# Kernel tuning notes

Measured on AMD Instinct MI355X. Metric: run time of the kernel, lower is better.

Reference implementation:

```python
import jax, jax.numpy as jnp
import numpy as np

N_NODES = 100000
N_EDGES = 1600000
IN_FEAT = 64
HIDDEN = 64
OUT_FEAT = 64
FCHIDDEN = 32
EMB_DIM = 20
FINAL_DIM = 2


def gcn_conv(x, W, b, src, dst, num_nodes):
    """PyG-style GCNConv: add self-loops, symmetric norm, linear, scatter-add."""
    loop = jnp.arange(num_nodes)
    s = jnp.concatenate([src, loop])  # message sources (x_j)
    d = jnp.concatenate([dst, loop])  # aggregation targets
    ones = jnp.ones(s.shape[0], dtype=x.dtype)
    deg = jax.ops.segment_sum(ones, d, num_segments=num_nodes)
    dinv = jnp.where(deg > 0, jax.lax.rsqrt(jnp.maximum(deg, 1.0)), 0.0)
    norm = dinv[s] * dinv[d]                      # [E+N]
    h = x @ W                                     # [N, out]
    msg = h[s] * norm[:, None]                    # gather + scale
    return jax.ops.segment_sum(msg, d, num_segments=num_nodes) + b


def setup_inputs() -> dict:
    key = jax.random.key(0)
    ks = jax.random.split(key, 12)
    x = jax.random.normal(ks[0], (N_NODES, IN_FEAT), dtype=jnp.float32)
    edge_index = jax.random.randint(ks[1], (2, N_EDGES), 0, N_NODES, dtype=jnp.int64)
    edge_attr = jax.random.randint(ks[2], (4, N_EDGES), 0, EMB_DIM, dtype=jnp.int64)
    def lin(k, fan_in, fan_out):
        bound = 1.0 / np.sqrt(fan_in)
        kw, kb = jax.random.split(k)
        W = jax.random.uniform(kw, (fan_in, fan_out), jnp.float32, -bound, bound)
        b = jax.random.uniform(kb, (fan_out,), jnp.float32, -bound, bound)
        return W, b
    W1, b1 = lin(ks[3], IN_FEAT, HIDDEN)
    W2, b2 = lin(ks[4], HIDDEN, OUT_FEAT)
    emb0 = jax.random.normal(ks[5], (EMB_DIM, FCHIDDEN), dtype=jnp.float32)
    emb1 = jax.random.normal(ks[6], (EMB_DIM, FCHIDDEN), dtype=jnp.float32)
    fc_in = OUT_FEAT + 2 * FCHIDDEN + 2
    fcW1, fcb1 = lin(ks[7], fc_in, FINAL_DIM)
    fcW2, fcb2 = lin(ks[8], FINAL_DIM, 2)
    return dict(x=x, edge_index=edge_index, edge_attr=edge_attr,
                W1=W1, b1=b1, W2=W2, b2=b2, emb0=emb0, emb1=emb1,
                fcW1=fcW1, fcb1=fcb1, fcW2=fcW2, fcb2=fcb2)


def reference(x, edge_index, edge_attr, W1, b1, W2, b2, emb0, emb1,
              fcW1, fcb1, fcW2, fcb2):
    num_nodes = x.shape[0]
    src, dst = edge_index[0], edge_index[1]
    h = jax.nn.relu(gcn_conv(x, W1, b1, src, dst, num_nodes))
    h = gcn_conv(h, W2, b2, src, dst, num_nodes)
    node2edge = h[src] - h[dst]                     # [E, outFeat]
    ea = edge_attr.T                                # [E, 4]
    vl = ea[:, :2].astype(jnp.float32)              # [E, 2]
    e0 = emb0[ea[:, 2]]                             # [E, fchidden]
    e1 = emb1[ea[:, 3]]                             # [E, fchidden]
    total = jnp.concatenate([node2edge, vl, e0, e1], axis=1)
    out = jax.nn.relu(total @ fcW1 + fcb1)          # dropout = identity (eval)
    out = out @ fcW2 + fcb2                         # [E, 2]
    return jax.nn.log_softmax(out, axis=1)
```

## Files before the change

kernel.cpp:

```cpp
#include <hip/hip_runtime.h>
#include <hip/hip_bf16.h>
#include <math.h>


typedef __hip_bfloat16 bf16;
#define NBLK 256

__global__ __launch_bounds__(256) void kA(const int* __restrict__ dst,
                                          int* __restrict__ cntm,
                                          int E, int chunk, int NB) {
    __shared__ int h[512];
    int blk = blockIdx.x;
    for (int i = threadIdx.x; i < NB; i += 256) h[i] = 0;
    __syncthreads();
    int lo = blk * chunk, hi = min(E, lo + chunk);
    for (int e = lo + threadIdx.x; e < hi; e += 256)
        atomicAdd(&h[dst[e] >> 8], 1);
    __syncthreads();
    for (int i = threadIdx.x; i < NB; i += 256)
        cntm[(size_t)i * NBLK + blk] = h[i];
}

__global__ void k_mscan1(int* __restrict__ a, int* __restrict__ part, int M) {
    __shared__ int s[256];
    int i = blockIdx.x * 256 + threadIdx.x;
    int v = (i < M) ? a[i] : 0;
    s[threadIdx.x] = v;
    int x = v;
    for (int off = 1; off < 256; off <<= 1) {
        __syncthreads();
        int add = (threadIdx.x >= off) ? s[threadIdx.x - off] : 0;
        __syncthreads();
        x += add;
        s[threadIdx.x] = x;
    }
    if (i < M) a[i] = x - v;
    __syncthreads();
    if (threadIdx.x == 255) part[blockIdx.x] = s[255];
}

__global__ __launch_bounds__(512) void k_scan2small(
        int* __restrict__ part, int B,
        const float* __restrict__ W2,
        const float* __restrict__ emb0, const float* __restrict__ emb1,
        const float* __restrict__ fcW1, const float* __restrict__ fcb1,
        const float* __restrict__ fcW2, const float* __restrict__ fcb2,
        float* __restrict__ U, float* __restrict__ E0t,
        float* __restrict__ E1t, float* __restrict__ C) {
    __shared__ int s[512];
    int t = threadIdx.x;
    int v = (t < B) ? part[t] : 0;
    s[t] = v;
    int x = v;
    for (int off = 1; off < 512; off <<= 1) {
        __syncthreads();
        int add = (t >= off) ? s[t - off] : 0;
        __syncthreads();
        x += add;
        s[t] = x;
    }
    if (t < B) part[t] = x - v;
    if (t < 128) {
        int i = t >> 1, c = t & 1;
        float sum = 0.f;
        for (int j = 0; j < 64; ++j) sum += W2[i * 64 + j] * fcW1[j * 2 + c];
        U[i * 2 + c] = sum;
    } else if (t < 168) {
        int i = (t - 128) >> 1, c = t & 1;
        float s0 = 0.f, s1 = 0.f;
        for (int k = 0; k < 32; ++k) {
            s0 += emb0[i * 32 + k] * fcW1[(66 + k) * 2 + c];
            s1 += emb1[i * 32 + k] * fcW1[(98 + k) * 2 + c];
        }
        E0t[i * 2 + c] = s0;
        E1t[i * 2 + c] = s1;
    } else if (t == 168) {
        C[0] = fcb1[0];  C[1] = fcb1[1];
        C[2] = fcW1[128]; C[3] = fcW1[129];
        C[4] = fcW1[130]; C[5] = fcW1[131];
        C[6] = fcW2[0];  C[7] = fcW2[1];
        C[8] = fcW2[2];  C[9] = fcW2[3];
        C[10] = fcb2[0]; C[11] = fcb2[1];
    }
}

__global__ __launch_bounds__(256) void kB(const int* __restrict__ src,
                                          const int* __restrict__ dst,
                                          const int* __restrict__ cntm,
                                          const int* __restrict__ part,
                                          int* __restrict__ pairs,
                                          int E, int chunk, int NB) {
    __shared__ int off[512];
    int blk = blockIdx.x;
    for (int i = threadIdx.x; i < NB; i += 256)
        off[i] = cntm[(size_t)i * NBLK + blk] + part[i];
    __syncthreads();
    int lo = blk * chunk, hi = min(E, lo + chunk);
    for (int e = lo + threadIdx.x; e < hi; e += 256) {
        int d = dst[e];
        int pos = atomicAdd(&off[d >> 8], 1);
        pairs[pos] = ((d & 255) << 17) | src[e];
    }
}

__global__ __launch_bounds__(256) void kC(const int* __restrict__ part,
                                          const int* __restrict__ pairs,
                                          int* __restrict__ col, int* __restrict__ rp,
                                          float* __restrict__ dinv,
                                          int N, int E, int NB) {
    __shared__ int cnt[256];
    __shared__ int s[256];
    int b = blockIdx.x, t = threadIdx.x;
    int n0 = b << 8;
    int nn = min(256, N - n0);
    int base = part[b];
    int end  = (b == NB - 1) ? E : part[b + 1];
    cnt[t] = 0;
    __syncthreads();
    for (int j = base + t; j < end; j += 256)
        atomicAdd(&cnt[pairs[j] >> 17], 1);
    __syncthreads();
    int v = cnt[t];
    if (t < nn) dinv[n0 + t] = rsqrtf((float)v + 1.0f);
    s[t] = v;
    int x = v;
    for (int off = 1; off < 256; off <<= 1) {
        __syncthreads();
        int add = (t >= off) ? s[t - off] : 0;
        __syncthreads();
        x += add;
        s[t] = x;
    }
    __syncthreads();
    int excl = x - v;
    if (t < nn) rp[n0 + t] = base + excl;
    cnt[t] = base + excl;
    __syncthreads();
    for (int j = base + t; j < end; j += 256) {
        int v2 = pairs[j];
        int pos = atomicAdd(&cnt[v2 >> 17], 1);
        col[pos] = v2 & 0x1FFFF;
    }
    if (b == NB - 1 && t == 0) rp[N] = E;
}

__global__ __launch_bounds__(256) void k_gemm1(const float* __restrict__ x,
                                               const float* __restrict__ W1,
                                               const float* __restrict__ dinv,
                                               bf16* __restrict__ xWs, int N) {
    __shared__ __align__(16) float xs[64][66];
    __shared__ __align__(16) float Ws[64][64];
    int tid = threadIdx.x;
    int n0 = blockIdx.x * 64;
    for (int i = tid; i < 4096; i += 256) Ws[i >> 6][i & 63] = W1[i];
    for (int i = tid; i < 4096; i += 256) {
        int node = i >> 6, k = i & 63;
        float v = (n0 + node < N) ? x[(size_t)(n0 + node) * 64 + k] : 0.f;
        xs[k][node] = v;
    }
    __syncthreads();
    int tr = tid >> 4;
    int tc = tid & 15;
    float acc[4][4] = {};
#pragma unroll 8
    for (int k = 0; k < 64; ++k) {
        float2 xa = *(const float2*)&xs[k][tr * 4];
        float2 xb = *(const float2*)&xs[k][tr * 4 + 2];
        float4 wv = *(const float4*)&Ws[k][tc * 4];
        acc[0][0] = fmaf(xa.x, wv.x, acc[0][0]);
        acc[0][1] = fmaf(xa.x, wv.y, acc[0][1]);
        acc[0][2] = fmaf(xa.x, wv.z, acc[0][2]);
        acc[0][3] = fmaf(xa.x, wv.w, acc[0][3]);
        acc[1][0] = fmaf(xa.y, wv.x, acc[1][0]);
        acc[1][1] = fmaf(xa.y, wv.y, acc[1][1]);
        acc[1][2] = fmaf(xa.y, wv.z, acc[1][2]);
        acc[1][3] = fmaf(xa.y, wv.w, acc[1][3]);
        acc[2][0] = fmaf(xb.x, wv.x, acc[2][0]);
        acc[2][1] = fmaf(xb.x, wv.y, acc[2][1]);
        acc[2][2] = fmaf(xb.x, wv.z, acc[2][2]);
        acc[2][3] = fmaf(xb.x, wv.w, acc[2][3]);
        acc[3][0] = fmaf(xb.y, wv.x, acc[3][0]);
        acc[3][1] = fmaf(xb.y, wv.y, acc[3][1]);
        acc[3][2] = fmaf(xb.y, wv.z, acc[3][2]);
        acc[3][3] = fmaf(xb.y, wv.w, acc[3][3]);
    }
#pragma unroll
    for (int i = 0; i < 4; ++i) {
        int node = n0 + tr * 4 + i;
        if (node < N) {
            float di = dinv[node];
            __hip_bfloat162 p0, p1;
            p0.x = __float2bfloat16(di * acc[i][0]);
            p0.y = __float2bfloat16(di * acc[i][1]);
            p1.x = __float2bfloat16(di * acc[i][2]);
            p1.y = __float2bfloat16(di * acc[i][3]);
            __hip_bfloat162* dst2 = (__hip_bfloat162*)&xWs[(size_t)node * 64 + tc * 4];
            dst2[0] = p0;
            dst2[1] = p1;
        }
    }
}

__global__ __launch_bounds__(256) void k_gather1(
        const bf16* __restrict__ xWs, const float* __restrict__ dinv,
        const int* __restrict__ rp, const int* __restrict__ col,
        const float* __restrict__ b1, const float* __restrict__ U,
        float* __restrict__ Qs, int N, int E) {
    int wid = blockIdx.x * 8 + (threadIdx.x >> 5);
    int c = threadIdx.x & 31;
    if (wid >= N) return;
    const __hip_bfloat162* xW2 = (const __hip_bfloat162*)xWs;
    __hip_bfloat162 sv = xW2[(size_t)wid * 32 + c];
    float ax = __bfloat162float(sv.x);
    float ay = __bfloat162float(sv.y);
    int beg = rp[wid], end = rp[wid + 1];
    for (int base = beg; base < end; base += 32) {
        int nn = min(32, end - base);
        int colv = col[min(base + c, E - 1)];
        int jj = 0;
        for (; jj + 8 <= nn; jj += 8) {
            int m0 = __shfl(colv, jj + 0, 32);
            int m1 = __shfl(colv, jj + 1, 32);
            int m2 = __shfl(colv, jj + 2, 32);
            int m3 = __shfl(colv, jj + 3, 32);
            int m4 = __shfl(colv, jj + 4, 32);
            int m5 = __shfl(colv, jj + 5, 32);
            int m6 = __shfl(colv, jj + 6, 32);
            int m7 = __shfl(colv, jj + 7, 32);
            __hip_bfloat162 v0 = xW2[(size_t)m0 * 32 + c];
            __hip_bfloat162 v1 = xW2[(size_t)m1 * 32 + c];
            __hip_bfloat162 v2 = xW2[(size_t)m2 * 32 + c];
            __hip_bfloat162 v3 = xW2[(size_t)m3 * 32 + c];
            __hip_bfloat162 v4 = xW2[(size_t)m4 * 32 + c];
            __hip_bfloat162 v5 = xW2[(size_t)m5 * 32 + c];
            __hip_bfloat162 v6 = xW2[(size_t)m6 * 32 + c];
            __hip_bfloat162 v7 = xW2[(size_t)m7 * 32 + c];
            ax += __bfloat162float(v0.x); ay += __bfloat162float(v0.y);
            ax += __bfloat162float(v1.x); ay += __bfloat162float(v1.y);
            ax += __bfloat162float(v2.x); ay += __bfloat162float(v2.y);
            ax += __bfloat162float(v3.x); ay += __bfloat162float(v3.y);
            ax += __bfloat162float(v4.x); ay += __bfloat162float(v4.y);
            ax += __bfloat162float(v5.x); ay += __bfloat162float(v5.y);
            ax += __bfloat162float(v6.x); ay += __bfloat162float(v6.y);
            ax += __bfloat162float(v7.x); ay += __bfloat162float(v7.y);
        }
        for (; jj < nn; ++jj) {
            int m = __shfl(colv, jj, 32);
            __hip_bfloat162 v = xW2[(size_t)m * 32 + c];
            ax += __bfloat162float(v.x);
            ay += __bfloat162float(v.y);
        }
    }
    float di = dinv[wid];
    float2 b1v = ((const float2*)b1)[c];
    float h0 = fmaxf(fmaf(di, ax, b1v.x), 0.f);
    float h1 = fmaxf(fmaf(di, ay, b1v.y), 0.f);
    float4 Uv = ((const float4*)U)[c];
    float q0 = fmaf(h0, Uv.x, h1 * Uv.z);
    float q1 = fmaf(h0, Uv.y, h1 * Uv.w);
#pragma unroll
    for (int mm = 16; mm; mm >>= 1) {
        q0 += __shfl_xor(q0, mm);
        q1 += __shfl_xor(q1, mm);
    }
    if (c == 0) {
        Qs[2 * wid + 0] = di * q0;
        Qs[2 * wid + 1] = di * q1;
    }
}

__global__ void k_gather2(const float* __restrict__ dinv, const int* __restrict__ rp,
                          const int* __restrict__ col, const float* __restrict__ Qs,
                          float* __restrict__ P, int N) {
    int n = blockIdx.x * blockDim.x + threadIdx.x;
    if (n >= N) return;
    float2 self = ((const float2*)Qs)[n];
    float p0 = self.x, p1 = self.y;
    int beg = rp[n], end = rp[n + 1];
    int j = beg;
    for (; j + 4 <= end; j += 4) {
        int m0 = col[j + 0], m1 = col[j + 1], m2 = col[j + 2], m3 = col[j + 3];
        float2 q0 = ((const float2*)Qs)[m0];
        float2 q1 = ((const float2*)Qs)[m1];
        float2 q2 = ((const float2*)Qs)[m2];
        float2 q3 = ((const float2*)Qs)[m3];
        p0 += (q0.x + q1.x) + (q2.x + q3.x);
        p1 += (q0.y + q1.y) + (q2.y + q3.y);
    }
    for (; j < end; ++j) {
        float2 q = ((const float2*)Qs)[col[j]];
        p0 += q.x;
        p1 += q.y;
    }
    float di = dinv[n];
    P[2 * n + 0] = di * p0;
    P[2 * n + 1] = di * p1;
}

__global__ void k_edge(const int* __restrict__ src, const int* __restrict__ dst,
                       const int* __restrict__ attr, const float* __restrict__ P,
                       const float* __restrict__ E0t, const float* __restrict__ E1t,
                       const float* __restrict__ C, float* __restrict__ out, int E) {
    int e = blockIdx.x * blockDim.x + threadIdx.x;
    if (e >= E) return;
    int s = src[e], d = dst[e];
    float a0 = (float)attr[e];
    float a1 = (float)attr[E + e];
    int i2 = attr[2 * E + e], i3 = attr[3 * E + e];
    const float2* P2 = (const float2*)P;
    float2 ps = P2[s], pd = P2[d];
    float z0 = ps.x - pd.x + a0 * C[2] + a1 * C[4] + E0t[i2 * 2 + 0] + E1t[i3 * 2 + 0] + C[0];
    float z1 = ps.y - pd.y + a0 * C[3] + a1 * C[5] + E0t[i2 * 2 + 1] + E1t[i3 * 2 + 1] + C[1];
    float r0 = fmaxf(z0, 0.f), r1 = fmaxf(z1, 0.f);
    float o0 = r0 * C[6] + r1 * C[8] + C[10];
    float o1 = r0 * C[7] + r1 * C[9] + C[11];
    float m = fmaxf(o0, o1);
    float lse = m + logf(expf(o0 - m) + expf(o1 - m));
    float2 res;
    res.x = o0 - lse;
    res.y = o1 - lse;
    ((float2*)out)[e] = res;
}

extern "C" void kernel_launch(void* const* d_in, const int* in_sizes, int n_in,
                              void* d_out, int out_size, void* d_ws, size_t ws_size,
                              hipStream_t stream) {
    const float* x    = (const float*)d_in[0];
    const int*   ei   = (const int*)d_in[1];
    const int*   ea   = (const int*)d_in[2];
    const float* W1   = (const float*)d_in[3];
    const float* b1   = (const float*)d_in[4];
    const float* W2   = (const float*)d_in[5];
    const float* emb0 = (const float*)d_in[7];
    const float* emb1 = (const float*)d_in[8];
    const float* fcW1 = (const float*)d_in[9];
    const float* fcb1 = (const float*)d_in[10];
    const float* fcW2 = (const float*)d_in[11];
    const float* fcb2 = (const float*)d_in[12];

    const int N = in_sizes[0] / 64;
    const int E = in_sizes[1] / 2;
    const int* src = ei;
    const int* dst = ei + E;
    const int NB = (N + 255) >> 8;
    const int NBB = NB * NBLK;
    const int chunk = (E + NBLK - 1) / NBLK;
    const int BS = (NBB + 255) / 256;

    char* wsb = (char*)d_ws;
    float* dinv = (float*)wsb;
    int*   rp   = (int*)(wsb + (size_t)4 * 100352);
    int*   cntm = (int*)(wsb + (size_t)4 * 200704);
    int*   part = (int*)(wsb + (size_t)4 * 300800);
    float* U    = (float*)(wsb + (size_t)4 * 301312);
    float* E0t  = U + 128;
    float* E1t  = E0t + 40;
    float* C    = E1t + 40;
    float* Qs   = (float*)(wsb + (size_t)4 * 301568);
    float* P    = (float*)(wsb + (size_t)4 * 501760);
    bf16*  xWs  = (bf16*)(wsb + (size_t)4 * 702464);
    int*   col   = (int*)d_out;
    int*   pairs = (int*)d_out + E;

    kA<<<NBLK, 256, 0, stream>>>(dst, cntm, E, chunk, NB);
    k_mscan1<<<BS, 256, 0, stream>>>(cntm, part, NBB);
    k_scan2small<<<1, 512, 0, stream>>>(part, BS, W2, emb0, emb1, fcW1, fcb1,
                                        fcW2, fcb2, U, E0t, E1t, C);
    kB<<<NBLK, 256, 0, stream>>>(src, dst, cntm, part, pairs, E, chunk, NB);
    kC<<<NB, 256, 0, stream>>>(part, pairs, col, rp, dinv, N, E, NB);
    k_gemm1<<<(N + 63) / 64, 256, 0, stream>>>(x, W1, dinv, xWs, N);
    k_gather1<<<(N + 7) / 8, 256, 0, stream>>>(xWs, dinv, rp, col, b1, U, Qs, N, E);
    k_gather2<<<(N + 255) / 256, 256, 0, stream>>>(dinv, rp, col, Qs, P, N);
    k_edge<<<(E + 255) / 256, 256, 0, stream>>>(src, dst, ea, P, E0t, E1t, C,
                                                (float*)d_out, E);
}
```

Baseline: 257.1 us.

## Replace two-level bucket CSR build with global-atomic degree count and scatter

Replaces the block-histogram bucket sort (kA/kB/kC with a pairs staging buffer) with a direct CSR build: global atomic degree count, a per-node scan, a fixup kernel that also computes dinv and initialises cursors, and an atomic scatter of src into col. This removes the intermediate pairs pass and the local-sort kernel but relies on heavily contended global atomics on random destinations. Column order within a row becomes nondeterministic, and the cursor array reuses the Qs buffer before gather1 writes it.

New measurement: 404.0 us. 1.57x slower.

```diff
diff --git a/kernel.cpp b/kernel.cpp
--- a/kernel.cpp
+++ b/kernel.cpp
@@ -4,27 +4,19 @@
 
 
 typedef __hip_bfloat16 bf16;
-#define NBLK 256
-
-__global__ __launch_bounds__(256) void kA(const int* __restrict__ dst,
-                                          int* __restrict__ cntm,
-                                          int E, int chunk, int NB) {
-    __shared__ int h[512];
-    int blk = blockIdx.x;
-    for (int i = threadIdx.x; i < NB; i += 256) h[i] = 0;
-    __syncthreads();
-    int lo = blk * chunk, hi = min(E, lo + chunk);
-    for (int e = lo + threadIdx.x; e < hi; e += 256)
-        atomicAdd(&h[dst[e] >> 8], 1);
-    __syncthreads();
-    for (int i = threadIdx.x; i < NB; i += 256)
-        cntm[(size_t)i * NBLK + blk] = h[i];
-}
-
-__global__ void k_mscan1(int* __restrict__ a, int* __restrict__ part, int M) {
+
+__global__ __launch_bounds__(256) void k_deg(const int* __restrict__ dst,
+                                             int* __restrict__ deg, int E) {
+    int e = blockIdx.x * 256 + threadIdx.x;
+    if (e < E) atomicAdd(&deg[dst[e]], 1);
+}
+
+__global__ __launch_bounds__(256) void k_scan_deg(const int* __restrict__ deg,
+                                                  int* __restrict__ rp,
+                                                  int* __restrict__ part, int M) {
     __shared__ int s[256];
     int i = blockIdx.x * 256 + threadIdx.x;
-    int v = (i < M) ? a[i] : 0;
+    int v = (i < M) ? deg[i] : 0;
     s[threadIdx.x] = v;
     int x = v;
     for (int off = 1; off < 256; off <<= 1) {
@@ -34,7 +26,7 @@
         x += add;
         s[threadIdx.x] = x;
     }
-    if (i < M) a[i] = x - v;
+    if (i < M) rp[i] = x - v;
     __syncthreads();
     if (threadIdx.x == 255) part[blockIdx.x] = s[255];
 }
@@ -84,64 +76,32 @@
     }
 }
 
-__global__ __launch_bounds__(256) void kB(const int* __restrict__ src,
-                                          const int* __restrict__ dst,
-                                          const int* __restrict__ cntm,
-                                          const int* __restrict__ part,
-                                          int* __restrict__ pairs,
-                                          int E, int chunk, int NB) {
-    __shared__ int off[512];
-    int blk = blockIdx.x;
-    for (int i = threadIdx.x; i < NB; i += 256)
-        off[i] = cntm[(size_t)i * NBLK + blk] + part[i];
-    __syncthreads();
-    int lo = blk * chunk, hi = min(E, lo + chunk);
-    for (int e = lo + threadIdx.x; e < hi; e += 256) {
-        int d = dst[e];
-        int pos = atomicAdd(&off[d >> 8], 1);
-        pairs[pos] = ((d & 255) << 17) | src[e];
-    }
-}
-
-__global__ __launch_bounds__(256) void kC(const int* __restrict__ part,
-                                          const int* __restrict__ pairs,
-                                          int* __restrict__ col, int* __restrict__ rp,
-                                          float* __restrict__ dinv,
-                                          int N, int E, int NB) {
-    __shared__ int cnt[256];
-    __shared__ int s[256];
-    int b = blockIdx.x, t = threadIdx.x;
-    int n0 = b << 8;
-    int nn = min(256, N - n0);
-    int base = part[b];
-    int end  = (b == NB - 1) ? E : part[b + 1];
-    cnt[t] = 0;
-    __syncthreads();
-    for (int j = base + t; j < end; j += 256)
-        atomicAdd(&cnt[pairs[j] >> 17], 1);
-    __syncthreads();
-    int v = cnt[t];
-    if (t < nn) dinv[n0 + t] = rsqrtf((float)v + 1.0f);
-    s[t] = v;
-    int x = v;
-    for (int off = 1; off < 256; off <<= 1) {
-        __syncthreads();
-        int add = (t >= off) ? s[t - off] : 0;
-        __syncthreads();
-        x += add;
-        s[t] = x;
-    }
-    __syncthreads();
-    int excl = x - v;
-    if (t < nn) rp[n0 + t] = base + excl;
-    cnt[t] = base + excl;
-    __syncthreads();
-    for (int j = base + t; j < end; j += 256) {
-        int v2 = pairs[j];
-        int pos = atomicAdd(&cnt[v2 >> 17], 1);
-        col[pos] = v2 & 0x1FFFF;
-    }
-    if (b == NB - 1 && t == 0) rp[N] = E;
+__global__ __launch_bounds__(256) void k_fix(int* __restrict__ rp,
+                                             const int* __restrict__ part,
+                                             const int* __restrict__ deg,
+                                             int* __restrict__ cursor,
+                                             float* __restrict__ dinv,
+                                             int N, int E) {
+    int n = blockIdx.x * 256 + threadIdx.x;
+    if (n < N) {
+        int base = rp[n] + part[n >> 8];
+        rp[n] = base;
+        cursor[n] = base;
+        dinv[n] = rsqrtf((float)deg[n] + 1.0f);
+    }
+    if (n == 0) rp[N] = E;
+}
+
+__global__ __launch_bounds__(256) void k_scatter(const int* __restrict__ src,
+                                                 const int* __restrict__ dst,
+                                                 int* __restrict__ cursor,
+                                                 int* __restrict__ col, int E) {
+    int e = blockIdx.x * 256 + threadIdx.x;
+    if (e >= E) return;
+    int d = dst[e];
+    int s = src[e];
+    int pos = atomicAdd(&cursor[d], 1);
+    col[pos] = s;
 }
 
 __global__ __launch_bounds__(256) void k_gemm1(const float* __restrict__ x,
@@ -342,32 +302,30 @@
     const int E = in_sizes[1] / 2;
     const int* src = ei;
     const int* dst = ei + E;
-    const int NB = (N + 255) >> 8;
-    const int NBB = NB * NBLK;
-    const int chunk = (E + NBLK - 1) / NBLK;
-    const int BS = (NBB + 255) / 256;
+    const int BS = (N + 255) / 256;
 
     char* wsb = (char*)d_ws;
     float* dinv = (float*)wsb;
     int*   rp   = (int*)(wsb + (size_t)4 * 100352);
-    int*   cntm = (int*)(wsb + (size_t)4 * 200704);
+    int*   deg  = (int*)(wsb + (size_t)4 * 200704);
     int*   part = (int*)(wsb + (size_t)4 * 300800);
     float* U    = (float*)(wsb + (size_t)4 * 301312);
     float* E0t  = U + 128;
     float* E1t  = E0t + 40;
     float* C    = E1t + 40;
     float* Qs   = (float*)(wsb + (size_t)4 * 301568);
+    int*   cursor = (int*)Qs;
     float* P    = (float*)(wsb + (size_t)4 * 501760);
     bf16*  xWs  = (bf16*)(wsb + (size_t)4 * 702464);
-    int*   col   = (int*)d_out;
-    int*   pairs = (int*)d_out + E;
-
-    kA<<<NBLK, 256, 0, stream>>>(dst, cntm, E, chunk, NB);
-    k_mscan1<<<BS, 256, 0, stream>>>(cntm, part, NBB);
+    int*   col  = (int*)d_out;
+
+    hipMemsetAsync(deg, 0, (size_t)N * 4, stream);
+    k_deg<<<(E + 255) / 256, 256, 0, stream>>>(dst, deg, E);
+    k_scan_deg<<<BS, 256, 0, stream>>>(deg, rp, part, N);
     k_scan2small<<<1, 512, 0, stream>>>(part, BS, W2, emb0, emb1, fcW1, fcb1,
                                         fcW2, fcb2, U, E0t, E1t, C);
-    kB<<<NBLK, 256, 0, stream>>>(src, dst, cntm, part, pairs, E, chunk, NB);
-    kC<<<NB, 256, 0, stream>>>(part, pairs, col, rp, dinv, N, E, NB);
+    k_fix<<<BS, 256, 0, stream>>>(rp, part, deg, cursor, dinv, N, E);
+    k_scatter<<<(E + 255) / 256, 256, 0, stream>>>(src, dst, cursor, col, E);
     k_gemm1<<<(N + 63) / 64, 256, 0, stream>>>(x, W1, dinv, xWs, N);
     k_gather1<<<(N + 7) / 8, 256, 0, stream>>>(xWs, dinv, rp, col, b1, U, Qs, N, E);
     k_gather2<<<(N + 255) / 256, 256, 0, stream>>>(dinv, rp, col, Qs, P, N);
```

## Fuse CSR build and first GEMM into one persistent kernel with grid barriers

Applied to the files above, without the earlier changes.

Six kernels (histogram, two-level scan, bucket scatter, per-bucket sort, GEMM1) are merged into a single persistent 256-block kernel that uses atomic-flag grid barriers between phases, with shared memory held in a union. This is meant to remove kernel launch gaps and tail effects between the small build stages. In exchange, the GEMM now runs on only 256 blocks looping over tiles (less parallelism), one block does the small scan alone, and the kernel depends on all 256 blocks being co-resident to avoid deadlock. A memset of the barrier flags is added.

Result: slower. 565.6 us (+120.0%).

```diff
diff --git a/kernel.cpp b/kernel.cpp
--- a/kernel.cpp
+++ b/kernel.cpp
@@ -6,197 +6,229 @@
 typedef __hip_bfloat16 bf16;
 #define NBLK 256
 
-__global__ __launch_bounds__(256) void kA(const int* __restrict__ dst,
-                                          int* __restrict__ cntm,
-                                          int E, int chunk, int NB) {
-    __shared__ int h[512];
-    int blk = blockIdx.x;
-    for (int i = threadIdx.x; i < NB; i += 256) h[i] = 0;
+__device__ __forceinline__ void gbar(int* flag) {
     __syncthreads();
-    int lo = blk * chunk, hi = min(E, lo + chunk);
-    for (int e = lo + threadIdx.x; e < hi; e += 256)
-        atomicAdd(&h[dst[e] >> 8], 1);
+    __threadfence();
+    if (threadIdx.x == 0) {
+        atomicAdd(flag, 1);
+        while (atomicAdd(flag, 0) < NBLK)
+            __builtin_amdgcn_s_sleep(2);
+    }
     __syncthreads();
-    for (int i = threadIdx.x; i < NB; i += 256)
-        cntm[(size_t)i * NBLK + blk] = h[i];
-}
-
-__global__ void k_mscan1(int* __restrict__ a, int* __restrict__ part, int M) {
-    __shared__ int s[256];
-    int i = blockIdx.x * 256 + threadIdx.x;
-    int v = (i < M) ? a[i] : 0;
-    s[threadIdx.x] = v;
-    int x = v;
-    for (int off = 1; off < 256; off <<= 1) {
-        __syncthreads();
-        int add = (threadIdx.x >= off) ? s[threadIdx.x - off] : 0;
-        __syncthreads();
-        x += add;
-        s[threadIdx.x] = x;
-    }
-    if (i < M) a[i] = x - v;
-    __syncthreads();
-    if (threadIdx.x == 255) part[blockIdx.x] = s[255];
-}
-
-__global__ __launch_bounds__(512) void k_scan2small(
-        int* __restrict__ part, int B,
+    __threadfence();
+}
+
+__global__ __launch_bounds__(256) void k_build(
+        const int* __restrict__ src, const int* __restrict__ dst,
+        const float* __restrict__ x, const float* __restrict__ W1,
         const float* __restrict__ W2,
         const float* __restrict__ emb0, const float* __restrict__ emb1,
         const float* __restrict__ fcW1, const float* __restrict__ fcb1,
         const float* __restrict__ fcW2, const float* __restrict__ fcb2,
+        int* __restrict__ cntm, int* __restrict__ part,
         float* __restrict__ U, float* __restrict__ E0t,
-        float* __restrict__ E1t, float* __restrict__ C) {
-    __shared__ int s[512];
-    int t = threadIdx.x;
-    int v = (t < B) ? part[t] : 0;
-    s[t] = v;
-    int x = v;
-    for (int off = 1; off < 512; off <<= 1) {
-        __syncthreads();
-        int add = (t >= off) ? s[t - off] : 0;
-        __syncthreads();
-        x += add;
-        s[t] = x;
-    }
-    if (t < B) part[t] = x - v;
-    if (t < 128) {
-        int i = t >> 1, c = t & 1;
-        float sum = 0.f;
-        for (int j = 0; j < 64; ++j) sum += W2[i * 64 + j] * fcW1[j * 2 + c];
-        U[i * 2 + c] = sum;
-    } else if (t < 168) {
-        int i = (t - 128) >> 1, c = t & 1;
-        float s0 = 0.f, s1 = 0.f;
-        for (int k = 0; k < 32; ++k) {
-            s0 += emb0[i * 32 + k] * fcW1[(66 + k) * 2 + c];
-            s1 += emb1[i * 32 + k] * fcW1[(98 + k) * 2 + c];
-        }
-        E0t[i * 2 + c] = s0;
-        E1t[i * 2 + c] = s1;
-    } else if (t == 168) {
-        C[0] = fcb1[0];  C[1] = fcb1[1];
-        C[2] = fcW1[128]; C[3] = fcW1[129];
-        C[4] = fcW1[130]; C[5] = fcW1[131];
-        C[6] = fcW2[0];  C[7] = fcW2[1];
-        C[8] = fcW2[2];  C[9] = fcW2[3];
-        C[10] = fcb2[0]; C[11] = fcb2[1];
-    }
-}
-
-__global__ __launch_bounds__(256) void kB(const int* __restrict__ src,
-                                          const int* __restrict__ dst,
-                                          const int* __restrict__ cntm,
-                                          const int* __restrict__ part,
-                                          int* __restrict__ pairs,
-                                          int E, int chunk, int NB) {
-    __shared__ int off[512];
-    int blk = blockIdx.x;
-    for (int i = threadIdx.x; i < NB; i += 256)
-        off[i] = cntm[(size_t)i * NBLK + blk] + part[i];
+        float* __restrict__ E1t, float* __restrict__ C,
+        int* __restrict__ pairs, int* __restrict__ col,
+        int* __restrict__ rp, float* __restrict__ dinv,
+        bf16* __restrict__ xWs, int* __restrict__ flags,
+        int N, int E, int NB, int chunk) {
+    __shared__ __align__(16) union {
+        struct { int h[512]; } p1;
+        struct { int s[256]; } p2;
+        struct { int s[256]; } p3;
+        struct { int off[512]; } p4;
+        struct { int cnt[256]; int s[256]; } p5;
+        struct { float xs[64][66]; float Ws[64][64]; } p6;
+    } sh;
+    const int b = blockIdx.x;
+    const int t = threadIdx.x;
+    const int lo = b * chunk, hi = min(E, lo + chunk);
+
+    for (int i = t; i < NB; i += 256) sh.p1.h[i] = 0;
     __syncthreads();
-    int lo = blk * chunk, hi = min(E, lo + chunk);
-    for (int e = lo + threadIdx.x; e < hi; e += 256) {
+    for (int e = lo + t; e < hi; e += 256)
+        atomicAdd(&sh.p1.h[dst[e] >> 8], 1);
+    __syncthreads();
+    for (int i = t; i < NB; i += 256)
+        cntm[(size_t)i * NBLK + b] = sh.p1.h[i];
+
+    gbar(flags + 0);
+
+    for (int r = b; r < NB; r += NBLK) {
+        int idx = (r << 8) + t;
+        int v = cntm[idx];
+        sh.p2.s[t] = v;
+        int xx = v;
+        for (int off = 1; off < 256; off <<= 1) {
+            __syncthreads();
+            int add = (t >= off) ? sh.p2.s[t - off] : 0;
+            __syncthreads();
+            xx += add;
+            sh.p2.s[t] = xx;
+        }
+        cntm[idx] = xx - v;
+        if (t == 255) part[r] = xx;
+        __syncthreads();
+    }
+    if (b == 192) {
+        if (t < 128) {
+            int i = t >> 1, c = t & 1;
+            float sum = 0.f;
+            for (int j = 0; j < 64; ++j) sum += W2[i * 64 + j] * fcW1[j * 2 + c];
+            U[i * 2 + c] = sum;
+        }
+    } else if (b == 193) {
+        if (t < 40) {
+            int i = t >> 1, c = t & 1;
+            float s0 = 0.f, s1 = 0.f;
+            for (int k = 0; k < 32; ++k) {
+                s0 += emb0[i * 32 + k] * fcW1[(66 + k) * 2 + c];
+                s1 += emb1[i * 32 + k] * fcW1[(98 + k) * 2 + c];
+            }
+            E0t[i * 2 + c] = s0;
+            E1t[i * 2 + c] = s1;
+        }
+    } else if (b == 194) {
+        if (t == 0) {
+            C[0] = fcb1[0];  C[1] = fcb1[1];
+            C[2] = fcW1[128]; C[3] = fcW1[129];
+            C[4] = fcW1[130]; C[5] = fcW1[131];
+            C[6] = fcW2[0];  C[7] = fcW2[1];
+            C[8] = fcW2[2];  C[9] = fcW2[3];
+            C[10] = fcb2[0]; C[11] = fcb2[1];
+        }
+    }
+
+    gbar(flags + 1);
+
+    if (b == 0) {
+        int v2 = (256 + t < NB) ? part[256 + t] : 0;
+        int v1 = (t < NB) ? part[t] : 0;
+        sh.p3.s[t] = v1;
+        int x1 = v1;
+        for (int off = 1; off < 256; off <<= 1) {
+            __syncthreads();
+            int add = (t >= off) ? sh.p3.s[t - off] : 0;
+            __syncthreads();
+            x1 += add;
+            sh.p3.s[t] = x1;
+        }
+        __syncthreads();
+        int tot1 = sh.p3.s[255];
+        if (t < NB) part[t] = x1 - v1;
+        __syncthreads();
+        sh.p3.s[t] = v2;
+        int x2 = v2;
+        for (int off = 1; off < 256; off <<= 1) {
+            __syncthreads();
+            int add = (t >= off) ? sh.p3.s[t - off] : 0;
+            __syncthreads();
+            x2 += add;
+            sh.p3.s[t] = x2;
+        }
+        if (256 + t < NB) part[256 + t] = tot1 + (x2 - v2);
+    }
+
+    gbar(flags + 2);
+
+    for (int i = t; i < NB; i += 256)
+        sh.p4.off[i] = cntm[(size_t)i * NBLK + b] + part[i];
+    __syncthreads();
+    for (int e = lo + t; e < hi; e += 256) {
         int d = dst[e];
-        int pos = atomicAdd(&off[d >> 8], 1);
+        int pos = atomicAdd(&sh.p4.off[d >> 8], 1);
         pairs[pos] = ((d & 255) << 17) | src[e];
     }
-}
-
-__global__ __launch_bounds__(256) void kC(const int* __restrict__ part,
-                                          const int* __restrict__ pairs,
-                                          int* __restrict__ col, int* __restrict__ rp,
-                                          float* __restrict__ dinv,
-                                          int N, int E, int NB) {
-    __shared__ int cnt[256];
-    __shared__ int s[256];
-    int b = blockIdx.x, t = threadIdx.x;
-    int n0 = b << 8;
-    int nn = min(256, N - n0);
-    int base = part[b];
-    int end  = (b == NB - 1) ? E : part[b + 1];
-    cnt[t] = 0;
-    __syncthreads();
-    for (int j = base + t; j < end; j += 256)
-        atomicAdd(&cnt[pairs[j] >> 17], 1);
-    __syncthreads();
-    int v = cnt[t];
-    if (t < nn) dinv[n0 + t] = rsqrtf((float)v + 1.0f);
-    s[t] = v;
-    int x = v;
-    for (int off = 1; off < 256; off <<= 1) {
-        __syncthreads();
-        int add = (t >= off) ? s[t - off] : 0;
-        __syncthreads();
-        x += add;
-        s[t] = x;
-    }
-    __syncthreads();
-    int excl = x - v;
-    if (t < nn) rp[n0 + t] = base + excl;
-    cnt[t] = base + excl;
-    __syncthreads();
-    for (int j = base + t; j < end; j += 256) {
-        int v2 = pairs[j];
-        int pos = atomicAdd(&cnt[v2 >> 17], 1);
-        col[pos] = v2 & 0x1FFFF;
-    }
-    if (b == NB - 1 && t == 0) rp[N] = E;
-}
-
-__global__ __launch_bounds__(256) void k_gemm1(const float* __restrict__ x,
-                                               const float* __restrict__ W1,
-                                               const float* __restrict__ dinv,
-                                               bf16* __restrict__ xWs, int N) {
-    __shared__ __align__(16) float xs[64][66];
-    __shared__ __align__(16) float Ws[64][64];
-    int tid = threadIdx.x;
-    int n0 = blockIdx.x * 64;
-    for (int i = tid; i < 4096; i += 256) Ws[i >> 6][i & 63] = W1[i];
-    for (int i = tid; i < 4096; i += 256) {
-        int node = i >> 6, k = i & 63;
-        float v = (n0 + node < N) ? x[(size_t)(n0 + node) * 64 + k] : 0.f;
-        xs[k][node] = v;
-    }
-    __syncthreads();
-    int tr = tid >> 4;
-    int tc = tid & 15;
-    float acc[4][4] = {};
+
+    gbar(flags + 3);
+
+    for (int bb = b; bb < NB; bb += NBLK) {
+        __syncthreads();
+        int n0 = bb << 8;
+        int nn = min(256, N - n0);
+        int base = part[bb];
+        int end  = (bb == NB - 1) ? E : part[bb + 1];
+        sh.p5.cnt[t] = 0;
+        __syncthreads();
+        for (int j = base + t; j < end; j += 256)
+            atomicAdd(&sh.p5.cnt[pairs[j] >> 17], 1);
+        __syncthreads();
+        int v = sh.p5.cnt[t];
+        if (t < nn) dinv[n0 + t] = rsqrtf((float)v + 1.0f);
+        sh.p5.s[t] = v;
+        int xx = v;
+        for (int off = 1; off < 256; off <<= 1) {
+            __syncthreads();
+            int add = (t >= off) ? sh.p5.s[t - off] : 0;
+            __syncthreads();
+            xx += add;
+            sh.p5.s[t] = xx;
+        }
+        __syncthreads();
+        int excl = xx - v;
+        if (t < nn) rp[n0 + t] = base + excl;
+        sh.p5.cnt[t] = base + excl;
+        __syncthreads();
+        for (int j = base + t; j < end; j += 256) {
+            int v2 = pairs[j];
+            int pos = atomicAdd(&sh.p5.cnt[v2 >> 17], 1);
+            col[pos] = v2 & 0x1FFFF;
+        }
+        if (bb == NB - 1 && t == 0) rp[N] = E;
+    }
+
+    gbar(flags + 4);
+
+    int ntiles = (N + 63) >> 6;
+    for (int tile = b; tile < ntiles; tile += NBLK) {
+        __syncthreads();
+        int n0 = tile << 6;
+        for (int i = t; i < 4096; i += 256) sh.p6.Ws[i >> 6][i & 63] = W1[i];
+        for (int i = t; i < 4096; i += 256) {
+            int node = i >> 6, k = i & 63;
+            float v = (n0 + node < N) ? x[(size_t)(n0 + node) * 64 + k] : 0.f;
+            sh.p6.xs[k][node] = v;
+        }
+        __syncthreads();
+        int tr = t >> 4;
+        int tc = t & 15;
+        float acc[4][4] = {};
 #pragma unroll 8
-    for (int k = 0; k < 64; ++k) {
-        float2 xa = *(const float2*)&xs[k][tr * 4];
-        float2 xb = *(const float2*)&xs[k][tr * 4 + 2];
-        float4 wv = *(const float4*)&Ws[k][tc * 4];
-        acc[0][0] = fmaf(xa.x, wv.x, acc[0][0]);
-        acc[0][1] = fmaf(xa.x, wv.y, acc[0][1]);
-        acc[0][2] = fmaf(xa.x, wv.z, acc[0][2]);
-        acc[0][3] = fmaf(xa.x, wv.w, acc[0][3]);
-        acc[1][0] = fmaf(xa.y, wv.x, acc[1][0]);
-        acc[1][1] = fmaf(xa.y, wv.y, acc[1][1]);
-        acc[1][2] = fmaf(xa.y, wv.z, acc[1][2]);
-        acc[1][3] = fmaf(xa.y, wv.w, acc[1][3]);
-        acc[2][0] = fmaf(xb.x, wv.x, acc[2][0]);
-        acc[2][1] = fmaf(xb.x, wv.y, acc[2][1]);
-        acc[2][2] = fmaf(xb.x, wv.z, acc[2][2]);
-        acc[2][3] = fmaf(xb.x, wv.w, acc[2][3]);
-        acc[3][0] = fmaf(xb.y, wv.x, acc[3][0]);
-        acc[3][1] = fmaf(xb.y, wv.y, acc[3][1]);
-        acc[3][2] = fmaf(xb.y, wv.z, acc[3][2]);
-        acc[3][3] = fmaf(xb.y, wv.w, acc[3][3]);
-    }
+        for (int k = 0; k < 64; ++k) {
+            float2 xa = *(const float2*)&sh.p6.xs[k][tr * 4];
+            float2 xb = *(const float2*)&sh.p6.xs[k][tr * 4 + 2];
+            float4 wv = *(const float4*)&sh.p6.Ws[k][tc * 4];
+            acc[0][0] = fmaf(xa.x, wv.x, acc[0][0]);
+            acc[0][1] = fmaf(xa.x, wv.y, acc[0][1]);
+            acc[0][2] = fmaf(xa.x, wv.z, acc[0][2]);
+            acc[0][3] = fmaf(xa.x, wv.w, acc[0][3]);
+            acc[1][0] = fmaf(xa.y, wv.x, acc[1][0]);
+            acc[1][1] = fmaf(xa.y, wv.y, acc[1][1]);
+            acc[1][2] = fmaf(xa.y, wv.z, acc[1][2]);
+            acc[1][3] = fmaf(xa.y, wv.w, acc[1][3]);
+            acc[2][0] = fmaf(xb.x, wv.x, acc[2][0]);
+            acc[2][1] = fmaf(xb.x, wv.y, acc[2][1]);
+            acc[2][2] = fmaf(xb.x, wv.z, acc[2][2]);
+            acc[2][3] = fmaf(xb.x, wv.w, acc[2][3]);
+            acc[3][0] = fmaf(xb.y, wv.x, acc[3][0]);
+            acc[3][1] = fmaf(xb.y, wv.y, acc[3][1]);
+            acc[3][2] = fmaf(xb.y, wv.z, acc[3][2]);
+            acc[3][3] = fmaf(xb.y, wv.w, acc[3][3]);
+        }
 #pragma unroll
-    for (int i = 0; i < 4; ++i) {
-        int node = n0 + tr * 4 + i;
-        if (node < N) {
-            float di = dinv[node];
-            __hip_bfloat162 p0, p1;
-            p0.x = __float2bfloat16(di * acc[i][0]);
-            p0.y = __float2bfloat16(di * acc[i][1]);
-            p1.x = __float2bfloat16(di * acc[i][2]);
-            p1.y = __float2bfloat16(di * acc[i][3]);
-            __hip_bfloat162* dst2 = (__hip_bfloat162*)&xWs[(size_t)node * 64 + tc * 4];
-            dst2[0] = p0;
-            dst2[1] = p1;
+        for (int i = 0; i < 4; ++i) {
+            int node = n0 + tr * 4 + i;
+            if (node < N) {
+                float di = dinv[node];
+                __hip_bfloat162 p0, p1;
+                p0.x = __float2bfloat16(di * acc[i][0]);
+                p0.y = __float2bfloat16(di * acc[i][1]);
+                p1.x = __float2bfloat16(di * acc[i][2]);
+                p1.y = __float2bfloat16(di * acc[i][3]);
+                __hip_bfloat162* dst2 = (__hip_bfloat162*)&xWs[(size_t)node * 64 + tc * 4];
+                dst2[0] = p0;
+                dst2[1] = p1;
+            }
         }
     }
 }
@@ -338,14 +370,12 @@
     const float* fcW2 = (const float*)d_in[11];
     const float* fcb2 = (const float*)d_in[12];
 
-    const int N = in_sizes[0] / 64;
-    const int E = in_sizes[1] / 2;
+    int N = in_sizes[0] / 64;
+    int E = in_sizes[1] / 2;
     const int* src = ei;
     const int* dst = ei + E;
-    const int NB = (N + 255) >> 8;
-    const int NBB = NB * NBLK;
-    const int chunk = (E + NBLK - 1) / NBLK;
-    const int BS = (NBB + 255) / 256;
+    int NB = (N + 255) >> 8;
+    int chunk = (E + NBLK - 1) / NBLK;
 
     char* wsb = (char*)d_ws;
     float* dinv = (float*)wsb;
@@ -356,19 +386,18 @@
     float* E0t  = U + 128;
     float* E1t  = E0t + 40;
     float* C    = E1t + 40;
+    int*   flags = (int*)(wsb + (size_t)4 * 301536);
     float* Qs   = (float*)(wsb + (size_t)4 * 301568);
     float* P    = (float*)(wsb + (size_t)4 * 501760);
     bf16*  xWs  = (bf16*)(wsb + (size_t)4 * 702464);
     int*   col   = (int*)d_out;
     int*   pairs = (int*)d_out + E;
 
-    kA<<<NBLK, 256, 0, stream>>>(dst, cntm, E, chunk, NB);
-    k_mscan1<<<BS, 256, 0, stream>>>(cntm, part, NBB);
-    k_scan2small<<<1, 512, 0, stream>>>(part, BS, W2, emb0, emb1, fcW1, fcb1,
-                                        fcW2, fcb2, U, E0t, E1t, C);
-    kB<<<NBLK, 256, 0, stream>>>(src, dst, cntm, part, pairs, E, chunk, NB);
-    kC<<<NB, 256, 0, stream>>>(part, pairs, col, rp, dinv, N, E, NB);
-    k_gemm1<<<(N + 63) / 64, 256, 0, stream>>>(x, W1, dinv, xWs, N);
+    hipMemsetAsync(flags, 0, 32, stream);
+    k_build<<<NBLK, 256, 0, stream>>>(
+        src, dst, x, W1, W2, emb0, emb1, fcW1, fcb1, fcW2, fcb2,
+        cntm, part, U, E0t, E1t, C, pairs, col, rp, dinv, xWs, flags,
+        N, E, NB, chunk);
     k_gather1<<<(N + 7) / 8, 256, 0, stream>>>(xWs, dinv, rp, col, b1, U, Qs, N, E);
     k_gather2<<<(N + 255) / 256, 256, 0, stream>>>(dinv, rp, col, Qs, P, N);
     k_edge<<<(E + 255) / 256, 256, 0, stream>>>(src, dst, ea, P, E0t, E1t, C,
```

## Fold small scan and weight precompute into neighbor kernels, fuse CSR build with GEMM1

Applied to the files above, without the earlier changes.

Removes the single-block scan kernel: the block-partial scan is now redone redundantly in every kB block, and the small weight-folding precompute moves into three spare kA blocks. The CSR finalisation kernel kC is fused with the first GEMM, so each 256-node block computes dinv and then its own 4 GEMM tiles with shared memory reused via a union. Together these cut two launches and their serialization gaps. The cost is redundant scan work per kB block and far fewer blocks for the GEMM (NB instead of N/64), which lowers its parallelism.

New measurement: 285.3 us. 10.9% more time.

```diff
diff --git a/kernel.cpp b/kernel.cpp
--- a/kernel.cpp
+++ b/kernel.cpp
@@ -7,18 +7,58 @@
 #define NBLK 256
 
 __global__ __launch_bounds__(256) void kA(const int* __restrict__ dst,
+                                          const float* __restrict__ W2,
+                                          const float* __restrict__ emb0,
+                                          const float* __restrict__ emb1,
+                                          const float* __restrict__ fcW1,
+                                          const float* __restrict__ fcb1,
+                                          const float* __restrict__ fcW2,
+                                          const float* __restrict__ fcb2,
                                           int* __restrict__ cntm,
+                                          float* __restrict__ U,
+                                          float* __restrict__ E0t,
+                                          float* __restrict__ E1t,
+                                          float* __restrict__ C,
                                           int E, int chunk, int NB) {
     __shared__ int h[512];
     int blk = blockIdx.x;
-    for (int i = threadIdx.x; i < NB; i += 256) h[i] = 0;
+    int t = threadIdx.x;
+    for (int i = t; i < NB; i += 256) h[i] = 0;
     __syncthreads();
     int lo = blk * chunk, hi = min(E, lo + chunk);
-    for (int e = lo + threadIdx.x; e < hi; e += 256)
+    for (int e = lo + t; e < hi; e += 256)
         atomicAdd(&h[dst[e] >> 8], 1);
     __syncthreads();
-    for (int i = threadIdx.x; i < NB; i += 256)
+    for (int i = t; i < NB; i += 256)
         cntm[(size_t)i * NBLK + blk] = h[i];
+    if (blk == 192) {
+        if (t < 128) {
+            int i = t >> 1, c = t & 1;
+            float sum = 0.f;
+            for (int j = 0; j < 64; ++j) sum += W2[i * 64 + j] * fcW1[j * 2 + c];
+            U[i * 2 + c] = sum;
+        }
+    } else if (blk == 193) {
+        if (t < 40) {
+            int i = t >> 1, c = t & 1;
+            float s0 = 0.f, s1 = 0.f;
+            for (int k = 0; k < 32; ++k) {
+                s0 += emb0[i * 32 + k] * fcW1[(66 + k) * 2 + c];
+                s1 += emb1[i * 32 + k] * fcW1[(98 + k) * 2 + c];
+            }
+            E0t[i * 2 + c] = s0;
+            E1t[i * 2 + c] = s1;
+        }
+    } else if (blk == 194) {
+        if (t == 0) {
+            C[0] = fcb1[0];  C[1] = fcb1[1];
+            C[2] = fcW1[128]; C[3] = fcW1[129];
+            C[4] = fcW1[130]; C[5] = fcW1[131];
+            C[6] = fcW2[0];  C[7] = fcW2[1];
+            C[8] = fcW2[2];  C[9] = fcW2[3];
+            C[10] = fcb2[0]; C[11] = fcb2[1];
+        }
+    }
 }
 
 __global__ void k_mscan1(int* __restrict__ a, int* __restrict__ part, int M) {
@@ -39,164 +79,153 @@
     if (threadIdx.x == 255) part[blockIdx.x] = s[255];
 }
 
-__global__ __launch_bounds__(512) void k_scan2small(
-        int* __restrict__ part, int B,
-        const float* __restrict__ W2,
-        const float* __restrict__ emb0, const float* __restrict__ emb1,
-        const float* __restrict__ fcW1, const float* __restrict__ fcb1,
-        const float* __restrict__ fcW2, const float* __restrict__ fcb2,
-        float* __restrict__ U, float* __restrict__ E0t,
-        float* __restrict__ E1t, float* __restrict__ C) {
-    __shared__ int s[512];
-    int t = threadIdx.x;
-    int v = (t < B) ? part[t] : 0;
-    s[t] = v;
-    int x = v;
-    for (int off = 1; off < 512; off <<= 1) {
-        __syncthreads();
-        int add = (t >= off) ? s[t - off] : 0;
-        __syncthreads();
-        x += add;
-        s[t] = x;
-    }
-    if (t < B) part[t] = x - v;
-    if (t < 128) {
-        int i = t >> 1, c = t & 1;
-        float sum = 0.f;
-        for (int j = 0; j < 64; ++j) sum += W2[i * 64 + j] * fcW1[j * 2 + c];
-        U[i * 2 + c] = sum;
-    } else if (t < 168) {
-        int i = (t - 128) >> 1, c = t & 1;
-        float s0 = 0.f, s1 = 0.f;
-        for (int k = 0; k < 32; ++k) {
-            s0 += emb0[i * 32 + k] * fcW1[(66 + k) * 2 + c];
-            s1 += emb1[i * 32 + k] * fcW1[(98 + k) * 2 + c];
-        }
-        E0t[i * 2 + c] = s0;
-        E1t[i * 2 + c] = s1;
-    } else if (t == 168) {
-        C[0] = fcb1[0];  C[1] = fcb1[1];
-        C[2] = fcW1[128]; C[3] = fcW1[129];
-        C[4] = fcW1[130]; C[5] = fcW1[131];
-        C[6] = fcW2[0];  C[7] = fcW2[1];
-        C[8] = fcW2[2];  C[9] = fcW2[3];
-        C[10] = fcb2[0]; C[11] = fcb2[1];
-    }
-}
-
 __global__ __launch_bounds__(256) void kB(const int* __restrict__ src,
                                           const int* __restrict__ dst,
                                           const int* __restrict__ cntm,
                                           const int* __restrict__ part,
+                                          int* __restrict__ partS,
                                           int* __restrict__ pairs,
                                           int E, int chunk, int NB) {
-    __shared__ int off[512];
+    __shared__ int sc[256];
+    __shared__ int base[512];
     int blk = blockIdx.x;
-    for (int i = threadIdx.x; i < NB; i += 256)
-        off[i] = cntm[(size_t)i * NBLK + blk] + part[i];
+    int t = threadIdx.x;
+    int v2 = (256 + t < NB) ? part[256 + t] : 0;
+    int v1 = (t < NB) ? part[t] : 0;
+    sc[t] = v1;
+    int x1 = v1;
+    for (int off = 1; off < 256; off <<= 1) {
+        __syncthreads();
+        int add = (t >= off) ? sc[t - off] : 0;
+        __syncthreads();
+        x1 += add;
+        sc[t] = x1;
+    }
+    __syncthreads();
+    int tot1 = sc[255];
+    base[t] = x1 - v1;
+    __syncthreads();
+    sc[t] = v2;
+    int x2 = v2;
+    for (int off = 1; off < 256; off <<= 1) {
+        __syncthreads();
+        int add = (t >= off) ? sc[t - off] : 0;
+        __syncthreads();
+        x2 += add;
+        sc[t] = x2;
+    }
+    base[256 + t] = tot1 + (x2 - v2);
+    __syncthreads();
+    if (blk == 0) {
+        if (t < NB) partS[t] = base[t];
+        if (256 + t < NB) partS[256 + t] = base[256 + t];
+    }
+    for (int i = t; i < NB; i += 256)
+        base[i] += cntm[(size_t)i * NBLK + blk];
     __syncthreads();
     int lo = blk * chunk, hi = min(E, lo + chunk);
-    for (int e = lo + threadIdx.x; e < hi; e += 256) {
+    for (int e = lo + t; e < hi; e += 256) {
         int d = dst[e];
-        int pos = atomicAdd(&off[d >> 8], 1);
+        int pos = atomicAdd(&base[d >> 8], 1);
         pairs[pos] = ((d & 255) << 17) | src[e];
     }
 }
 
-__global__ __launch_bounds__(256) void kC(const int* __restrict__ part,
-                                          const int* __restrict__ pairs,
-                                          int* __restrict__ col, int* __restrict__ rp,
-                                          float* __restrict__ dinv,
-                                          int N, int E, int NB) {
-    __shared__ int cnt[256];
-    __shared__ int s[256];
+__global__ __launch_bounds__(256) void kCG(const int* __restrict__ partS,
+                                           const int* __restrict__ pairs,
+                                           const float* __restrict__ x,
+                                           const float* __restrict__ W1,
+                                           int* __restrict__ col, int* __restrict__ rp,
+                                           float* __restrict__ dinv,
+                                           bf16* __restrict__ xWs,
+                                           int N, int E, int NB) {
+    __shared__ __align__(16) union {
+        struct { int cnt[256]; int s[256]; } c;
+        struct { float xs[64][66]; float Ws[64][64]; } g;
+    } sh;
     int b = blockIdx.x, t = threadIdx.x;
     int n0 = b << 8;
     int nn = min(256, N - n0);
-    int base = part[b];
-    int end  = (b == NB - 1) ? E : part[b + 1];
-    cnt[t] = 0;
+    int base = partS[b];
+    int end  = (b == NB - 1) ? E : partS[b + 1];
+    sh.c.cnt[t] = 0;
     __syncthreads();
     for (int j = base + t; j < end; j += 256)
-        atomicAdd(&cnt[pairs[j] >> 17], 1);
-    __syncthreads();
-    int v = cnt[t];
+        atomicAdd(&sh.c.cnt[pairs[j] >> 17], 1);
+    __syncthreads();
+    int v = sh.c.cnt[t];
     if (t < nn) dinv[n0 + t] = rsqrtf((float)v + 1.0f);
-    s[t] = v;
-    int x = v;
+    sh.c.s[t] = v;
+    int xx = v;
     for (int off = 1; off < 256; off <<= 1) {
         __syncthreads();
-        int add = (t >= off) ? s[t - off] : 0;
-        __syncthreads();
-        x += add;
-        s[t] = x;
-    }
-    __syncthreads();
-    int excl = x - v;
+        int add = (t >= off) ? sh.c.s[t - off] : 0;
+        __syncthreads();
+        xx += add;
+        sh.c.s[t] = xx;
+    }
+    __syncthreads();
+    int excl = xx - v;
     if (t < nn) rp[n0 + t] = base + excl;
-    cnt[t] = base + excl;
+    sh.c.cnt[t] = base + excl;
     __syncthreads();
     for (int j = base + t; j < end; j += 256) {
         int v2 = pairs[j];
-        int pos = atomicAdd(&cnt[v2 >> 17], 1);
+        int pos = atomicAdd(&sh.c.cnt[v2 >> 17], 1);
         col[pos] = v2 & 0x1FFFF;
     }
     if (b == NB - 1 && t == 0) rp[N] = E;
-}
-
-__global__ __launch_bounds__(256) void k_gemm1(const float* __restrict__ x,
-                                               const float* __restrict__ W1,
-                                               const float* __restrict__ dinv,
-                                               bf16* __restrict__ xWs, int N) {
-    __shared__ __align__(16) float xs[64][66];
-    __shared__ __align__(16) float Ws[64][64];
-    int tid = threadIdx.x;
-    int n0 = blockIdx.x * 64;
-    for (int i = tid; i < 4096; i += 256) Ws[i >> 6][i & 63] = W1[i];
-    for (int i = tid; i < 4096; i += 256) {
-        int node = i >> 6, k = i & 63;
-        float v = (n0 + node < N) ? x[(size_t)(n0 + node) * 64 + k] : 0.f;
-        xs[k][node] = v;
-    }
-    __syncthreads();
-    int tr = tid >> 4;
-    int tc = tid & 15;
-    float acc[4][4] = {};
+
+    int tr = t >> 4;
+    int tc = t & 15;
+    for (int tile = 0; tile < 4; ++tile) {
+        int ng = n0 + (tile << 6);
+        if (ng >= N) break;
+        __syncthreads();
+        for (int i = t; i < 4096; i += 256) sh.g.Ws[i >> 6][i & 63] = W1[i];
+        for (int i = t; i < 4096; i += 256) {
+            int node = i >> 6, k = i & 63;
+            float vv = (ng + node < N) ? x[(size_t)(ng + node) * 64 + k] : 0.f;
+            sh.g.xs[k][node] = vv;
+        }
+        __syncthreads();
+        float acc[4][4] = {};
 #pragma unroll 8
-    for (int k = 0; k < 64; ++k) {
-        float2 xa = *(const float2*)&xs[k][tr * 4];
-        float2 xb = *(const float2*)&xs[k][tr * 4 + 2];
-        float4 wv = *(const float4*)&Ws[k][tc * 4];
-        acc[0][0] = fmaf(xa.x, wv.x, acc[0][0]);
-        acc[0][1] = fmaf(xa.x, wv.y, acc[0][1]);
-        acc[0][2] = fmaf(xa.x, wv.z, acc[0][2]);
-        acc[0][3] = fmaf(xa.x, wv.w, acc[0][3]);
-        acc[1][0] = fmaf(xa.y, wv.x, acc[1][0]);
-        acc[1][1] = fmaf(xa.y, wv.y, acc[1][1]);
-        acc[1][2] = fmaf(xa.y, wv.z, acc[1][2]);
-        acc[1][3] = fmaf(xa.y, wv.w, acc[1][3]);
-        acc[2][0] = fmaf(xb.x, wv.x, acc[2][0]);
-        acc[2][1] = fmaf(xb.x, wv.y, acc[2][1]);
-        acc[2][2] = fmaf(xb.x, wv.z, acc[2][2]);
-        acc[2][3] = fmaf(xb.x, wv.w, acc[2][3]);
-        acc[3][0] = fmaf(xb.y, wv.x, acc[3][0]);
-        acc[3][1] = fmaf(xb.y, wv.y, acc[3][1]);
-        acc[3][2] = fmaf(xb.y, wv.z, acc[3][2]);
-        acc[3][3] = fmaf(xb.y, wv.w, acc[3][3]);
-    }
+        for (int k = 0; k < 64; ++k) {
+            float2 xa = *(const float2*)&sh.g.xs[k][tr * 4];
+            float2 xb = *(const float2*)&sh.g.xs[k][tr * 4 + 2];
+            float4 wv = *(const float4*)&sh.g.Ws[k][tc * 4];
+            acc[0][0] = fmaf(xa.x, wv.x, acc[0][0]);
+            acc[0][1] = fmaf(xa.x, wv.y, acc[0][1]);
+            acc[0][2] = fmaf(xa.x, wv.z, acc[0][2]);
+            acc[0][3] = fmaf(xa.x, wv.w, acc[0][3]);
+            acc[1][0] = fmaf(xa.y, wv.x, acc[1][0]);
+            acc[1][1] = fmaf(xa.y, wv.y, acc[1][1]);
+            acc[1][2] = fmaf(xa.y, wv.z, acc[1][2]);
+            acc[1][3] = fmaf(xa.y, wv.w, acc[1][3]);
+            acc[2][0] = fmaf(xb.x, wv.x, acc[2][0]);
+            acc[2][1] = fmaf(xb.x, wv.y, acc[2][1]);
+            acc[2][2] = fmaf(xb.x, wv.z, acc[2][2]);
+            acc[2][3] = fmaf(xb.x, wv.w, acc[2][3]);
+            acc[3][0] = fmaf(xb.y, wv.x, acc[3][0]);
+            acc[3][1] = fmaf(xb.y, wv.y, acc[3][1]);
+            acc[3][2] = fmaf(xb.y, wv.z, acc[3][2]);
+            acc[3][3] = fmaf(xb.y, wv.w, acc[3][3]);
+        }
 #pragma unroll
-    for (int i = 0; i < 4; ++i) {
-        int node = n0 + tr * 4 + i;
-        if (node < N) {
-            float di = dinv[node];
-            __hip_bfloat162 p0, p1;
-            p0.x = __float2bfloat16(di * acc[i][0]);
-            p0.y = __float2bfloat16(di * acc[i][1]);
-            p1.x = __float2bfloat16(di * acc[i][2]);
-            p1.y = __float2bfloat16(di * acc[i][3]);
-            __hip_bfloat162* dst2 = (__hip_bfloat162*)&xWs[(size_t)node * 64 + tc * 4];
-            dst2[0] = p0;
-            dst2[1] = p1;
+        for (int i = 0; i < 4; ++i) {
+            int node = ng + tr * 4 + i;
+            if (node < N) {
+                float di = dinv[node];
+                __hip_bfloat162 p0, p1;
+                p0.x = __float2bfloat16(di * acc[i][0]);
+                p0.y = __float2bfloat16(di * acc[i][1]);
+                p1.x = __float2bfloat16(di * acc[i][2]);
+                p1.y = __float2bfloat16(di * acc[i][3]);
+                __hip_bfloat162* dst2 = (__hip_bfloat162*)&xWs[(size_t)node * 64 + tc * 4];
+                dst2[0] = p0;
+                dst2[1] = p1;
+            }
         }
     }
 }
@@ -359,16 +388,15 @@
     float* Qs   = (float*)(wsb + (size_t)4 * 301568);
     float* P    = (float*)(wsb + (size_t)4 * 501760);
     bf16*  xWs  = (bf16*)(wsb + (size_t)4 * 702464);
+    int*   partS = (int*)(wsb + (size_t)4 * 3902464);
     int*   col   = (int*)d_out;
     int*   pairs = (int*)d_out + E;
 
-    kA<<<NBLK, 256, 0, stream>>>(dst, cntm, E, chunk, NB);
+    kA<<<NBLK, 256, 0, stream>>>(dst, W2, emb0, emb1, fcW1, fcb1, fcW2, fcb2,
+                                 cntm, U, E0t, E1t, C, E, chunk, NB);
     k_mscan1<<<BS, 256, 0, stream>>>(cntm, part, NBB);
-    k_scan2small<<<1, 512, 0, stream>>>(part, BS, W2, emb0, emb1, fcW1, fcb1,
-                                        fcW2, fcb2, U, E0t, E1t, C);
-    kB<<<NBLK, 256, 0, stream>>>(src, dst, cntm, part, pairs, E, chunk, NB);
-    kC<<<NB, 256, 0, stream>>>(part, pairs, col, rp, dinv, N, E, NB);
-    k_gemm1<<<(N + 63) / 64, 256, 0, stream>>>(x, W1, dinv, xWs, N);
+    kB<<<NBLK, 256, 0, stream>>>(src, dst, cntm, part, partS, pairs, E, chunk, NB);
+    kCG<<<NB, 256, 0, stream>>>(partS, pairs, x, W1, col, rp, dinv, xWs, N, E, NB);
     k_gather1<<<(N + 7) / 8, 256, 0, stream>>>(xWs, dinv, rp, col, b1, U, Qs, N, E);
     k_gather2<<<(N + 255) / 256, 256, 0, stream>>>(dinv, rp, col, Qs, P, N);
     k_edge<<<(E + 255) / 256, 256, 0, stream>>>(src, dst, ea, P, E0t, E1t, C,
```
